# Kernel tuning notes

Measured on AMD Instinct MI355X. Metric: run time of the kernel, lower is better.

## Reference

```python
import jax, jax.numpy as jnp
import numpy as np

N = 100000
E = 1600000
D_IN = 64
D_HID = 64


def setup_inputs() -> dict:
    key = jax.random.key(0)
    k1, k2, k3 = jax.random.split(key, 3)
    x = jax.random.normal(k1, (N, D_IN), dtype=jnp.float32)
    edge_index = jax.random.randint(k2, (2, E), 0, N, dtype=jnp.int64)
    # GCNConv linear weight (Glorot-like scale) and bias (zeros at init)
    W = jax.random.normal(k3, (D_IN, D_HID), dtype=jnp.float32) * (1.0 / np.sqrt(D_IN))
    b = jnp.zeros((D_HID,), dtype=jnp.float32)
    return {"x": x, "edge_index": edge_index, "W": W, "b": b}


def gcn_conv(x, edge_index, W, b):
    n = x.shape[0]
    # dense projection first (PyG GCNConv applies lin before propagate)
    xw = x @ W  # [N, D_HID]
    # add self-loops
    loop = jnp.arange(n, dtype=edge_index.dtype)
    src = jnp.concatenate([edge_index[0], loop])  # [E + N]
    dst = jnp.concatenate([edge_index[1], loop])
    # symmetric degree normalization with self-loops, unit edge weights
    ones = jnp.ones(src.shape[0], dtype=xw.dtype)
    deg = jax.ops.segment_sum(ones, dst, num_segments=n)  # [N]
    dinv = jnp.where(deg > 0, jax.lax.rsqrt(deg), 0.0)
    norm = dinv[src] * dinv[dst]  # [E + N]
    # gather, scale, scatter-add
    msgs = xw[src] * norm[:, None]  # [E + N, D_HID]
    out = jax.ops.segment_sum(msgs, dst, num_segments=n)  # [N, D_HID]
    return out + b


def reference(x, edge_index, W, b):
    return gcn_conv(x, edge_index, W, b)
```

## Files before the change

### kernel.cpp

```cpp
#include <hip/hip_runtime.h>
#include <hip/hip_fp16.h>

#define NN 100000
#define NE 1600000
#define D 64
#define SPAN 512
#define NB 196
#define BCAP 10240
#define ECH 4096
#define NP1 ((NE + ECH - 1) / ECH)
#define RB 128
#define NXB ((NN + RB - 1) / RB)

__global__ void k_part(const int* __restrict__ src, const int* __restrict__ dst,
                       int* __restrict__ bcur, unsigned* __restrict__ brecs, int e) {
    __shared__ int hist[256];
    __shared__ int excl[256];
    __shared__ int cur[256];
    __shared__ int gbase[256];
    __shared__ unsigned stage[ECH];
    __shared__ unsigned char stgb[ECH];

    int tid = threadIdx.x;
    int e0  = blockIdx.x * ECH;
    int ecnt = min(ECH, e - e0);

    hist[tid] = 0;
    __syncthreads();

    for (int i = tid * 4; i < ecnt; i += 1024) {
        if (i + 3 < ecnt) {
            int4 d = *(const int4*)(dst + e0 + i);
            atomicAdd(&hist[d.x >> 9], 1);
            atomicAdd(&hist[d.y >> 9], 1);
            atomicAdd(&hist[d.z >> 9], 1);
            atomicAdd(&hist[d.w >> 9], 1);
        } else {
            for (int j = i; j < ecnt; ++j) atomicAdd(&hist[dst[e0 + j] >> 9], 1);
        }
    }
    __syncthreads();

    int v = hist[tid];
    excl[tid] = v;
    __syncthreads();
    for (int off = 1; off < 256; off <<= 1) {
        int t = (tid >= off) ? excl[tid - off] : 0;
        __syncthreads();
        excl[tid] += t;
        __syncthreads();
    }
    int ex = excl[tid] - v;
    __syncthreads();
    excl[tid] = ex;
    cur[tid]  = ex;
    if (v > 0) gbase[tid] = atomicAdd(&bcur[tid], v);
    __syncthreads();

    for (int i = tid * 4; i < ecnt; i += 1024) {
        if (i + 3 < ecnt) {
            int4 d = *(const int4*)(dst + e0 + i);
            int4 s = *(const int4*)(src + e0 + i);
            int bk; int p;
            bk = d.x >> 9; p = atomicAdd(&cur[bk], 1); stage[p] = ((unsigned)s.x << 9) | (unsigned)(d.x & 511); stgb[p] = (unsigned char)bk;
            bk = d.y >> 9; p = atomicAdd(&cur[bk], 1); stage[p] = ((unsigned)s.y << 9) | (unsigned)(d.y & 511); stgb[p] = (unsigned char)bk;
            bk = d.z >> 9; p = atomicAdd(&cur[bk], 1); stage[p] = ((unsigned)s.z << 9) | (unsigned)(d.z & 511); stgb[p] = (unsigned char)bk;
            bk = d.w >> 9; p = atomicAdd(&cur[bk], 1); stage[p] = ((unsigned)s.w << 9) | (unsigned)(d.w & 511); stgb[p] = (unsigned char)bk;
        } else {
            for (int j = i; j < ecnt; ++j) {
                int dd = dst[e0 + j], ss = src[e0 + j];
                int bk = dd >> 9;
                int p = atomicAdd(&cur[bk], 1);
                stage[p] = ((unsigned)ss << 9) | (unsigned)(dd & 511);
                stgb[p] = (unsigned char)bk;
            }
        }
    }
    __syncthreads();

    for (int i = tid; i < ecnt; i += 256) {
        unsigned rec = stage[i];
        int bk = stgb[i];
        int gp = gbase[bk] + (i - excl[bk]);
        if (gp < BCAP)
            brecs[(size_t)bk * BCAP + gp] = rec;
    }
}

__global__ void __launch_bounds__(512)
k_fine(const unsigned* __restrict__ brecs, const int* __restrict__ bcur,
       int* __restrict__ cnt, int* __restrict__ rowstart,
       int* __restrict__ recs2, int n) {
    __shared__ int lcnt[SPAN];
    __shared__ int lcur[SPAN];
    __shared__ int tmp[512];
    __shared__ int sh_bbase;

    int b   = blockIdx.x;
    int tid = threadIdx.x;

    lcnt[tid] = 0;

    tmp[tid] = (tid < NB) ? min(bcur[tid], BCAP) : 0;
    __syncthreads();
    for (int off = 1; off < 512; off <<= 1) {
        int u = (tid >= off) ? tmp[tid - off] : 0;
        __syncthreads();
        tmp[tid] += u;
        __syncthreads();
    }
    if (tid == 0) sh_bbase = (b == 0) ? 0 : tmp[b - 1];

    int nrec = min(bcur[b], BCAP);
    const unsigned* rb = brecs + (size_t)b * BCAP;

    for (int i = tid; i < nrec; i += 512)
        atomicAdd(&lcnt[rb[i] & 511], 1);
    __syncthreads();

    int v = lcnt[tid];
    tmp[tid] = v;
    __syncthreads();
    for (int off = 1; off < 512; off <<= 1) {
        int u = (tid >= off) ? tmp[tid - off] : 0;
        __syncthreads();
        tmp[tid] += u;
        __syncthreads();
    }
    int ex = tmp[tid] - v;
    lcur[tid] = ex;
    __syncthreads();

    int base = sh_bbase;
    int node = b * SPAN + tid;
    if (node < n) {
        cnt[node] = v;
        rowstart[node] = base + ex;
    }

    for (int i = tid; i < nrec; i += 512) {
        unsigned rec = rb[i];
        int dl = rec & 511;
        int p = atomicAdd(&lcur[dl], 1);
        recs2[base + p] = (int)(rec >> 9);
    }
}

__global__ void __launch_bounds__(128)
k_xw2h(const float* __restrict__ x, const float* __restrict__ W,
       const int* __restrict__ cnt, __half* __restrict__ xw2, int n) {
    __shared__ float sW[D][68];
    __shared__ float sx[RB][64];

    int tid = threadIdx.x;
    int w   = tid >> 6;
    int l   = tid & 63;
    int rg  = l >> 3;
    int cg  = l & 7;
    int rowbase = blockIdx.x * RB;

#pragma unroll
    for (int i = 0; i < 8; ++i) {
        int f = i * 128 + tid;
        int k = f >> 4, c4 = (f & 15) * 4;
        *(float4*)(&sW[k][c4]) = *(const float4*)(W + k * D + c4);
    }
#pragma unroll
    for (int i = 0; i < 16; ++i) {
        int f = i * 128 + tid;
        int row = f >> 4, kc = f & 15;
        int gr = rowbase + row; if (gr >= n) gr = n - 1;
        float4 v = *(const float4*)(x + (size_t)gr * D + kc * 4);
        int sc = kc ^ ((row >> 3) & 7);
        *(float4*)(&sx[row][sc * 4]) = v;
    }
    __syncthreads();

    int rb0 = w * 64 + rg * 8;
    float acc[8][8];
#pragma unroll
    for (int rr = 0; rr < 8; ++rr)
#pragma unroll
        for (int cc = 0; cc < 8; ++cc) acc[rr][cc] = 0.f;

    int swz = (rb0 >> 3) & 7;
    for (int ks = 0; ks < 16; ++ks) {
        float4 xv[8];
#pragma unroll
        for (int rr = 0; rr < 8; ++rr)
            xv[rr] = *(const float4*)(&sx[rb0 + rr][(ks ^ swz) * 4]);
#pragma unroll
        for (int j = 0; j < 4; ++j) {
            int k = ks * 4 + j;
            float4 w0 = *(const float4*)(&sW[k][cg * 8]);
            float4 w1 = *(const float4*)(&sW[k][cg * 8 + 4]);
#pragma unroll
            for (int rr = 0; rr < 8; ++rr) {
                float xs = (j == 0) ? xv[rr].x : (j == 1) ? xv[rr].y : (j == 2) ? xv[rr].z : xv[rr].w;
                acc[rr][0] += xs * w0.x;
                acc[rr][1] += xs * w0.y;
                acc[rr][2] += xs * w0.z;
                acc[rr][3] += xs * w0.w;
                acc[rr][4] += xs * w1.x;
                acc[rr][5] += xs * w1.y;
                acc[rr][6] += xs * w1.z;
                acc[rr][7] += xs * w1.w;
            }
        }
    }

    union H2U { __half2 h; unsigned u; };
#pragma unroll
    for (int rr = 0; rr < 8; ++rr) {
        int grow = rowbase + rb0 + rr;
        if (grow >= n) break;
        float di = rsqrtf((float)cnt[grow] + 1.0f);
        int4 pk;
        H2U a, bb, c, d;
        a.h  = __half2(__float2half_rn(acc[rr][0] * di), __float2half_rn(acc[rr][1] * di));
        bb.h = __half2(__float2half_rn(acc[rr][2] * di), __float2half_rn(acc[rr][3] * di));
        c.h  = __half2(__float2half_rn(acc[rr][4] * di), __float2half_rn(acc[rr][5] * di));
        d.h  = __half2(__float2half_rn(acc[rr][6] * di), __float2half_rn(acc[rr][7] * di));
        pk.x = (int)a.u; pk.y = (int)bb.u; pk.z = (int)c.u; pk.w = (int)d.u;
        *(int4*)(xw2 + (size_t)grow * D + cg * 8) = pk;
    }
}

__global__ void k_gather(const int* __restrict__ recs, const int* __restrict__ rowstart,
                         const int* __restrict__ cnt, const __half* __restrict__ xw2,
                         const float* __restrict__ b, float* __restrict__ out, int n) {
    int wid  = (blockIdx.x * blockDim.x + threadIdx.x) >> 6;
    if (wid >= n) return;
    int lane = threadIdx.x & 63;
    int eg   = lane >> 3;
    int cb   = lane & 7;

    int base = __builtin_amdgcn_readfirstlane(rowstart[wid]);
    int k    = __builtin_amdgcn_readfirstlane(cnt[wid]);

    float acc[8];
#pragma unroll
    for (int j = 0; j < 8; ++j) acc[j] = 0.f;

    for (int i0 = 0; i0 < k; i0 += 8) {
        int e = i0 + eg;
        if (e < k) {
            int s = recs[base + e];
            int4 v = *((const int4*)(xw2 + (size_t)s * D) + cb);
            const __half2* hp = (const __half2*)&v;
            float2 f0 = __half22float2(hp[0]);
            float2 f1 = __half22float2(hp[1]);
            float2 f2 = __half22float2(hp[2]);
            float2 f3 = __half22float2(hp[3]);
            acc[0] += f0.x; acc[1] += f0.y;
            acc[2] += f1.x; acc[3] += f1.y;
            acc[4] += f2.x; acc[5] += f2.y;
            acc[6] += f3.x; acc[7] += f3.y;
        }
    }

#pragma unroll
    for (int m = 8; m < 64; m <<= 1)
#pragma unroll
        for (int j = 0; j < 8; ++j)
            acc[j] += __shfl_xor(acc[j], m, 64);

    if (eg == 0) {
        float di = rsqrtf((float)k + 1.0f);
        int4 sv = *((const int4*)(xw2 + (size_t)wid * D) + cb);
        const __half2* sp = (const __half2*)&sv;
        float2 s0 = __half22float2(sp[0]);
        float2 s1 = __half22float2(sp[1]);
        float2 s2 = __half22float2(sp[2]);
        float2 s3 = __half22float2(sp[3]);
        float4 b0 = *(const float4*)(b + cb * 8);
        float4 b1 = *(const float4*)(b + cb * 8 + 4);
        float4 o0, o1;
        o0.x = (acc[0] + s0.x) * di + b0.x;
        o0.y = (acc[1] + s0.y) * di + b0.y;
        o0.z = (acc[2] + s1.x) * di + b0.z;
        o0.w = (acc[3] + s1.y) * di + b0.w;
        o1.x = (acc[4] + s2.x) * di + b1.x;
        o1.y = (acc[5] + s2.y) * di + b1.y;
        o1.z = (acc[6] + s3.x) * di + b1.z;
        o1.w = (acc[7] + s3.y) * di + b1.w;
        *(float4*)(out + (size_t)wid * D + cb * 8)     = o0;
        *(float4*)(out + (size_t)wid * D + cb * 8 + 4) = o1;
    }
}

extern "C" void kernel_launch(void* const* d_in, const int* in_sizes, int n_in,
                              void* d_out, int out_size, void* d_ws, size_t ws_size,
                              hipStream_t stream) {
    const float* x  = (const float*)d_in[0];
    const int*   ei = (const int*)d_in[1];
    const float* W  = (const float*)d_in[2];
    const float* b  = (const float*)d_in[3];
    float* out = (float*)d_out;

    __half*   xw2      = (__half*)d_ws;
    int*      cnt      = (int*)(xw2 + (size_t)NN * D);
    int*      rowstart = cnt + NN;
    int*      bcur     = rowstart + NN;
    unsigned* brecs    = (unsigned*)(bcur + NB);
    int*      recs2    = (int*)(brecs + (size_t)NB * BCAP);

    const int* src = ei;
    const int* dst = ei + NE;

    hipMemsetAsync(bcur, 0, NB * sizeof(int), stream);

    k_part <<<NP1, 256, 0, stream>>>(src, dst, bcur, brecs, NE);
    k_fine <<<NB, 512, 0, stream>>>(brecs, bcur, cnt, rowstart, recs2, NN);
    k_xw2h <<<NXB, 128, 0, stream>>>(x, W, cnt, xw2, NN);

    long long tot = (long long)NN * 64;
    k_gather<<<(int)((tot + 255) / 256), 256, 0, stream>>>(recs2, rowstart, cnt, xw2, b, out, NN);
}
```

Baseline: 114.9 us.

## Stage per-block CSR indices in LDS and unroll gather by two edges

```diff
diff --git a/kernel.cpp b/kernel.cpp
--- a/kernel.cpp
+++ b/kernel.cpp
@@ -11,6 +11,9 @@
 #define NP1 ((NE + ECH - 1) / ECH)
 #define RB 128
 #define NXB ((NN + RB - 1) / RB)
+#define GN 64
+#define GCAP 2048
+#define NGB ((NN + GN - 1) / GN)
 
 __global__ void k_part(const int* __restrict__ src, const int* __restrict__ dst,
                        int* __restrict__ bcur, unsigned* __restrict__ brecs, int e) {
@@ -226,66 +229,101 @@
     }
 }
 
-__global__ void k_gather(const int* __restrict__ recs, const int* __restrict__ rowstart,
-                         const int* __restrict__ cnt, const __half* __restrict__ xw2,
-                         const float* __restrict__ b, float* __restrict__ out, int n) {
-    int wid  = (blockIdx.x * blockDim.x + threadIdx.x) >> 6;
-    if (wid >= n) return;
-    int lane = threadIdx.x & 63;
+__global__ void __launch_bounds__(256)
+k_gather(const int* __restrict__ recs, const int* __restrict__ rowstart,
+         const int* __restrict__ cnt, const __half* __restrict__ xw2,
+         const float* __restrict__ b, float* __restrict__ out, int n) {
+    __shared__ int lrs[GN];
+    __shared__ int lcn[GN];
+    __shared__ int lrec[GCAP];
+    __shared__ int sh_tot;
+
+    int tid = threadIdx.x;
+    int n0  = blockIdx.x * GN;
+    int nn  = min(GN, n - n0);
+
+    if (tid < nn) {
+        lrs[tid] = rowstart[n0 + tid];
+        lcn[tid] = cnt[n0 + tid];
+    }
+    __syncthreads();
+    if (tid == 0) sh_tot = lrs[nn - 1] + lcn[nn - 1] - lrs[0];
+    __syncthreads();
+
+    int bb  = lrs[0];
+    int tot = sh_tot;
+    for (int i = tid; i < tot && i < GCAP; i += 256)
+        lrec[i] = recs[bb + i];
+    __syncthreads();
+
+    int w    = tid >> 6;
+    int lane = tid & 63;
     int eg   = lane >> 3;
     int cb   = lane & 7;
 
-    int base = __builtin_amdgcn_readfirstlane(rowstart[wid]);
-    int k    = __builtin_amdgcn_readfirstlane(cnt[wid]);
-
-    float acc[8];
-#pragma unroll
-    for (int j = 0; j < 8; ++j) acc[j] = 0.f;
-
-    for (int i0 = 0; i0 < k; i0 += 8) {
-        int e = i0 + eg;
-        if (e < k) {
-            int s = recs[base + e];
-            int4 v = *((const int4*)(xw2 + (size_t)s * D) + cb);
-            const __half2* hp = (const __half2*)&v;
-            float2 f0 = __half22float2(hp[0]);
-            float2 f1 = __half22float2(hp[1]);
-            float2 f2 = __half22float2(hp[2]);
-            float2 f3 = __half22float2(hp[3]);
-            acc[0] += f0.x; acc[1] += f0.y;
-            acc[2] += f1.x; acc[3] += f1.y;
-            acc[4] += f2.x; acc[5] += f2.y;
-            acc[6] += f3.x; acc[7] += f3.y;
-        }
-    }
-
-#pragma unroll
-    for (int m = 8; m < 64; m <<= 1)
-#pragma unroll
-        for (int j = 0; j < 8; ++j)
-            acc[j] += __shfl_xor(acc[j], m, 64);
-
-    if (eg == 0) {
-        float di = rsqrtf((float)k + 1.0f);
-        int4 sv = *((const int4*)(xw2 + (size_t)wid * D) + cb);
-        const __half2* sp = (const __half2*)&sv;
-        float2 s0 = __half22float2(sp[0]);
-        float2 s1 = __half22float2(sp[1]);
-        float2 s2 = __half22float2(sp[2]);
-        float2 s3 = __half22float2(sp[3]);
-        float4 b0 = *(const float4*)(b + cb * 8);
-        float4 b1 = *(const float4*)(b + cb * 8 + 4);
-        float4 o0, o1;
-        o0.x = (acc[0] + s0.x) * di + b0.x;
-        o0.y = (acc[1] + s0.y) * di + b0.y;
-        o0.z = (acc[2] + s1.x) * di + b0.z;
-        o0.w = (acc[3] + s1.y) * di + b0.w;
-        o1.x = (acc[4] + s2.x) * di + b1.x;
-        o1.y = (acc[5] + s2.y) * di + b1.y;
-        o1.z = (acc[6] + s3.x) * di + b1.z;
-        o1.w = (acc[7] + s3.y) * di + b1.w;
-        *(float4*)(out + (size_t)wid * D + cb * 8)     = o0;
-        *(float4*)(out + (size_t)wid * D + cb * 8 + 4) = o1;
+    for (int nl = w; nl < nn; nl += 4) {
+        int base_l = lrs[nl] - bb;
+        int k      = lcn[nl];
+
+        float acc[8];
+#pragma unroll
+        for (int j = 0; j < 8; ++j) acc[j] = 0.f;
+
+        for (int i0 = 0; i0 < k; i0 += 16) {
+            int e1 = i0 + eg;
+            int e2 = i0 + 8 + eg;
+            int4 v1 = make_int4(0, 0, 0, 0);
+            int4 v2 = make_int4(0, 0, 0, 0);
+            if (e1 < k) {
+                int idx = base_l + e1;
+                int s = (idx < GCAP) ? lrec[idx] : recs[bb + idx];
+                v1 = *((const int4*)(xw2 + (size_t)s * D) + cb);
+            }
+            if (e2 < k) {
+                int idx = base_l + e2;
+                int s = (idx < GCAP) ? lrec[idx] : recs[bb + idx];
+                v2 = *((const int4*)(xw2 + (size_t)s * D) + cb);
+            }
+            const __half2* h1 = (const __half2*)&v1;
+            const __half2* h2 = (const __half2*)&v2;
+#pragma unroll
+            for (int j = 0; j < 4; ++j) {
+                float2 f1 = __half22float2(h1[j]);
+                float2 f2 = __half22float2(h2[j]);
+                acc[2 * j]     += f1.x + f2.x;
+                acc[2 * j + 1] += f1.y + f2.y;
+            }
+        }
+
+#pragma unroll
+        for (int m = 8; m < 64; m <<= 1)
+#pragma unroll
+            for (int j = 0; j < 8; ++j)
+                acc[j] += __shfl_xor(acc[j], m, 64);
+
+        if (eg == 0) {
+            int node = n0 + nl;
+            float di = rsqrtf((float)k + 1.0f);
+            int4 sv = *((const int4*)(xw2 + (size_t)node * D) + cb);
+            const __half2* sp = (const __half2*)&sv;
+            float2 s0 = __half22float2(sp[0]);
+            float2 s1 = __half22float2(sp[1]);
+            float2 s2 = __half22float2(sp[2]);
+            float2 s3 = __half22float2(sp[3]);
+            float4 b0 = *(const float4*)(b + cb * 8);
+            float4 b1 = *(const float4*)(b + cb * 8 + 4);
+            float4 o0, o1;
+            o0.x = (acc[0] + s0.x) * di + b0.x;
+            o0.y = (acc[1] + s0.y) * di + b0.y;
+            o0.z = (acc[2] + s1.x) * di + b0.z;
+            o0.w = (acc[3] + s1.y) * di + b0.w;
+            o1.x = (acc[4] + s2.x) * di + b1.x;
+            o1.y = (acc[5] + s2.y) * di + b1.y;
+            o1.z = (acc[6] + s3.x) * di + b1.z;
+            o1.w = (acc[7] + s3.y) * di + b1.w;
+            *(float4*)(out + (size_t)node * D + cb * 8)     = o0;
+            *(float4*)(out + (size_t)node * D + cb * 8 + 4) = o1;
+        }
     }
 }
 
@@ -314,6 +352,5 @@
     k_fine <<<NB, 512, 0, stream>>>(brecs, bcur, cnt, rowstart, recs2, NN);
     k_xw2h <<<NXB, 128, 0, stream>>>(x, W, cnt, xw2, NN);
 
-    long long tot = (long long)NN * 64;
-    k_gather<<<(int)((tot + 255) / 256), 256, 0, stream>>>(recs2, rowstart, cnt, xw2, b, out, NN);
-}
+    k_gather<<<NGB, 256, 0, stream>>>(recs2, rowstart, cnt, xw2, b, out, NN);
+}
```

Measured after the change: 111.5 us. -3.0%, faster.
